# Optimization experiments

Measured on AMD Instinct MI355X. Metric: run time of the kernel, lower is better.

Reference implementation:

```python
import jax, jax.numpy as jnp
import numpy as np

N_Q, N_X, N_Z = 1024, 512, 512
N_PER = N_Q + N_X + N_Z        # 2048 nodes per graph
B = 16                          # graphs per batch
DEG = 16                        # avg in/out degree
E_PER = N_PER * DEG
N = B * N_PER                   # 32768 total nodes
E = B * E_PER                   # 524288 total edges
HID, HEADS, L = 128, 4, 3
DH = HID // HEADS               # 32 per-head dim
EPS = 1e-5


def setup_inputs() -> dict:
    key = jax.random.key(0)
    ks = jax.random.split(key, 10)
    # one-hot node-type features (qubit / X-stab / Z-stab), tiled over batch
    sn = jnp.zeros((N_PER, 3), jnp.float32)
    sn = sn.at[:N_Q, 0].set(1.0).at[N_Q:N_Q + N_X, 1].set(1.0).at[N_Q + N_X:, 2].set(1.0)
    x = jnp.tile(sn, (B, 1))  # [N,3]
    # random sparse edges, graph-local then offset (mimics dense_to_sparse + Batch)
    src = jax.random.randint(ks[0], (B, E_PER), 0, N_PER)
    dst = jax.random.randint(ks[1], (B, E_PER), 0, N_PER)
    off = (jnp.arange(B) * N_PER)[:, None]
    edge_src = (src + off).reshape(-1).astype(jnp.int32)
    edge_dst = (dst + off).reshape(-1).astype(jnp.int32)
    seg = jnp.repeat(jnp.arange(B, dtype=jnp.int32), N_PER)  # graph id per node
    s = 0.05
    return dict(
        x=x, edge_src=edge_src, edge_dst=edge_dst, seg=seg,
        in_w=jax.random.normal(ks[2], (3, HID)) * s, in_b=jnp.zeros((HID,)),
        qw=jax.random.normal(ks[3], (L, HID, HID)) * s, qb=jnp.zeros((L, HID)),
        kw=jax.random.normal(ks[4], (L, HID, HID)) * s, kb=jnp.zeros((L, HID)),
        vw=jax.random.normal(ks[5], (L, HID, HID)) * s, vb=jnp.zeros((L, HID)),
        sw=jax.random.normal(ks[6], (L, HID, HID)) * s, sb=jnp.zeros((L, HID)),
        fw=jax.random.normal(ks[7], (L, HID, HID)) * s, fb=jnp.zeros((L, HID)),
        ln_g=jnp.ones((L, HID)), ln_b=jnp.zeros((L, HID)),
    )


def _layer_norm(h, g, b):
    mu = jnp.mean(h, axis=-1, keepdims=True)
    var = jnp.mean(jnp.square(h - mu), axis=-1, keepdims=True)
    return (h - mu) * jax.lax.rsqrt(var + EPS) * g + b


def reference(x, edge_src, edge_dst, seg, in_w, in_b, qw, qb, kw, kb, vw, vb,
              sw, sb, fw, fb, ln_g, ln_b):
    scale = 1.0 / jnp.sqrt(jnp.float32(DH))
    h = x @ in_w + in_b  # [N,HID]
    for i in range(L):
        h_res = h
        # TransformerConv: per-edge multi-head attention (softmax over in-neighbors)
        q = (h @ qw[i] + qb[i]).reshape(N, HEADS, DH)
        k = (h @ kw[i] + kb[i]).reshape(N, HEADS, DH)
        v = (h @ vw[i] + vb[i]).reshape(N, HEADS, DH)
        logits = jnp.einsum('ehd,ehd->eh', q[edge_dst], k[edge_src]) * scale  # [E,H]
        m = jax.ops.segment_max(logits, edge_dst, num_segments=N)             # [N,H]
        e = jnp.exp(logits - m[edge_dst])
        z = jax.ops.segment_sum(e, edge_dst, num_segments=N)                  # [N,H]
        alpha = e / z[edge_dst]
        agg = jax.ops.segment_sum(alpha[:, :, None] * v[edge_src], edge_dst,
                                  num_segments=N).reshape(N, HID)
        h = agg + h @ sw[i] + sb[i]        # root/skip linear (root_weight=True)
        # dropout is a no-op in eval mode
        h = h + jax.nn.relu(h @ fw[i] + fb[i])   # FFN residual
        h = h + h_res                            # outer residual
        h = jax.nn.relu(_layer_norm(h, ln_g[i], ln_b[i]))
    # global_mean_pool over graphs
    tot = jax.ops.segment_sum(h, seg, num_segments=B)                       # [B,HID]
    cnt = jax.ops.segment_sum(jnp.ones((N, 1), h.dtype), seg, num_segments=B)
    return tot / cnt
```

## Files before the change

kernel.cpp:

```cpp
#include <hip/hip_runtime.h>
#include <hip/hip_bf16.h>

#define N_TOT 32768
#define E_TOT 524288
#define HID 128
#define B_GR 16
#define NPER 2048
#define LAYERS 3
#define EPSLN 1e-5f
#define ELLW 64
#define SCALE_L2E (0.17677669529663687f * 1.4426950408889634f)

typedef float f4 __attribute__((ext_vector_type(4)));
typedef short bf16x8 __attribute__((ext_vector_type(8)));
typedef unsigned short u16x4 __attribute__((ext_vector_type(4)));

__device__ __forceinline__ unsigned short f2bf_rne(float x) {
    unsigned u = __float_as_uint(x);
    unsigned r = (u + 0x7FFFu + ((u >> 16) & 1u)) >> 16;
    return (unsigned short)r;
}

__device__ __forceinline__ float bf2f(unsigned short u) {
    return __uint_as_float(((unsigned)u) << 16);
}

__device__ __forceinline__ void unpack8(uint4 w, float* f) {
    f[0] = __uint_as_float(w.x << 16); f[1] = __uint_as_float(w.x & 0xFFFF0000u);
    f[2] = __uint_as_float(w.y << 16); f[3] = __uint_as_float(w.y & 0xFFFF0000u);
    f[4] = __uint_as_float(w.z << 16); f[5] = __uint_as_float(w.z & 0xFFFF0000u);
    f[6] = __uint_as_float(w.w << 16); f[7] = __uint_as_float(w.w & 0xFFFF0000u);
}

__global__ __launch_bounds__(256) void k_zp(const float* __restrict__ qw, const float* __restrict__ kw,
                                            const float* __restrict__ vw, const float* __restrict__ sw,
                                            const float* __restrict__ fw, unsigned short* __restrict__ wt,
                                            int* __restrict__ cursor, float* __restrict__ outz) {
    if (blockIdx.x < 960) {
        int mid = blockIdx.x >> 6;
        int within = (blockIdx.x & 63) * 256 + threadIdx.x;
        int l = mid / 5, t = mid % 5;
        const float* src = (t == 0 ? qw : t == 1 ? kw : t == 2 ? vw : t == 3 ? sw : fw) + l * HID * HID;
        int c = within >> 7;
        int kk = within & 127;
        int k = kk ^ ((c & 7) << 3);
        float sc = (t == 0) ? SCALE_L2E : 1.0f;
        wt[mid * HID * HID + c * HID + kk] = f2bf_rne(src[k * HID + c] * sc);
    } else if (blockIdx.x < 992) {
        int i = (blockIdx.x - 960) * 256 + threadIdx.x;
        reinterpret_cast<int4*>(cursor)[i] = int4{0, 0, 0, 0};
    } else {
        f4 z4 = {0.f, 0.f, 0.f, 0.f};
        reinterpret_cast<f4*>(outz)[threadIdx.x * 2] = z4;
        reinterpret_cast<f4*>(outz)[threadIdx.x * 2 + 1] = z4;
    }
}

#define GEMM_COMPUTE_G(acc, AL, WG)                                                         \
    {                                                                                       \
        _Pragma("unroll")                                                                   \
        for (int ks = 0; ks < 4; ++ks) {                                                    \
            bf16x8 a0 = *reinterpret_cast<const bf16x8*>(                                   \
                &AL[wm * 32 + lr][(ks * 32 + lg * 8) ^ swz]);                               \
            bf16x8 a1 = *reinterpret_cast<const bf16x8*>(                                   \
                &AL[wm * 32 + 16 + lr][(ks * 32 + lg * 8) ^ swz]);                          \
            _Pragma("unroll")                                                               \
            for (int n = 0; n < 4; ++n) {                                                   \
                bf16x8 b = *reinterpret_cast<const bf16x8*>(                                \
                    (WG) + (wn * 64 + n * 16 + lr) * HID + ((ks * 32 + lg * 8) ^ swz));     \
                acc[0][n] = __builtin_amdgcn_mfma_f32_16x16x32_bf16(a0, b, acc[0][n], 0, 0, 0); \
                acc[1][n] = __builtin_amdgcn_mfma_f32_16x16x32_bf16(a1, b, acc[1][n], 0, 0, 0); \
            }                                                                               \
        }                                                                                   \
    }

#define ZERO_ACC(acc)                                                        \
    {                                                                        \
        _Pragma("unroll")                                                    \
        for (int m = 0; m < 2; ++m)                                          \
            _Pragma("unroll")                                                \
            for (int n = 0; n < 4; ++n) acc[m][n] = f4{0, 0, 0, 0};          \
    }

#define QKV_EPILOGUE(ACC, T_IDX)                                                            \
    {                                                                                       \
        _Pragma("unroll")                                                                   \
        for (int n = 0; n < 4; ++n) {                                                       \
            int col = wn * 64 + n * 16 + lr;                                                \
            float bs = biases[T_IDX][col];                                                  \
            if (T_IDX == 0) bs *= SCALE_L2E;                                                \
            unsigned short* outp = (T_IDX == 0) ? oq : okv + ((T_IDX == 2) ? 128 : 0);      \
            const size_t stride = (T_IDX == 0) ? HID : 256;                                 \
            _Pragma("unroll")                                                               \
            for (int m = 0; m < 2; ++m) {                                                   \
                _Pragma("unroll")                                                           \
                for (int r = 0; r < 4; ++r) {                                               \
                    int row = r0 + wm * 32 + m * 16 + lg * 4 + r;                           \
                    outp[(size_t)row * stride + col] = f2bf_rne(ACC[m][n][r] + bs);         \
                }                                                                           \
            }                                                                               \
        }                                                                                   \
    }

__global__ __launch_bounds__(256) void k_scatter_init(const int* __restrict__ esrc, const int* __restrict__ edst,
                                                      int* __restrict__ cursor, unsigned short* __restrict__ ell,
                                                      const float* __restrict__ x,
                                                      const float* __restrict__ in_w,
                                                      const float* __restrict__ in_b,
                                                      const unsigned short* __restrict__ wl,
                                                      const float* __restrict__ qb, const float* __restrict__ kb,
                                                      const float* __restrict__ vb,
                                                      unsigned short* __restrict__ h16,
                                                      unsigned short* __restrict__ oq,
                                                      unsigned short* __restrict__ okv) {
    __shared__ unsigned short A_lds[64][HID];
    int tid = threadIdx.x;
    if (blockIdx.x < E_TOT / 256) {
        int e = blockIdx.x * 256 + tid;
        int d = edst[e];
        int pos = atomicAdd(&cursor[d], 1);
        if (pos < ELLW) ell[d * ELLW + pos] = (unsigned short)esrc[e];
        return;
    }
    int r0 = (blockIdx.x - E_TOT / 256) * 64;
    int lane = tid & 63, w = tid >> 6;
    int wm = w >> 1, wn = w & 1;
    int lr = lane & 15, lg = lane >> 4;
    int swz = (lane & 7) << 3;

    #pragma unroll
    for (int p = 0; p < 8; ++p) {
        int idx = p * 256 + tid;
        int row = idx >> 5;
        int k0 = (idx & 31) * 4;
        int n = r0 + row;
        float x0 = x[n * 3 + 0], x1 = x[n * 3 + 1], x2 = x[n * 3 + 2];
        u16x4 b;
        #pragma unroll
        for (int i = 0; i < 4; ++i) {
            int c = k0 + i;
            b[i] = f2bf_rne(x0 * in_w[c] + x1 * in_w[HID + c] + x2 * in_w[2 * HID + c] + in_b[c]);
        }
        int cs = k0 ^ ((row & 7) << 3);
        *reinterpret_cast<u16x4*>(&A_lds[row][cs]) = b;
        *reinterpret_cast<u16x4*>(&h16[(size_t)n * HID + cs]) = b;
    }
    __syncthreads();

    const float* biases[3] = {qb, kb, vb};
    f4 acc[2][4];
    #pragma unroll
    for (int t = 0; t < 3; ++t) {
        ZERO_ACC(acc);
        GEMM_COMPUTE_G(acc, A_lds, wl + t * HID * HID);
        QKV_EPILOGUE(acc, t);
    }
}

__global__ __launch_bounds__(256) void k_attn5(const unsigned short* __restrict__ qb16,
                                               const unsigned short* __restrict__ kv16,
                                               const int* __restrict__ deg,
                                               const unsigned short* __restrict__ ell,
                                               unsigned short* __restrict__ outagg) {
    int bid = blockIdx.x;
    int xcd = bid & 7;
    int chunk = bid >> 3;
    int g2 = xcd + 8 * (chunk >> 9);
    int nb = g2 * 512 + (chunk & 511);
    int n = nb * 4 + (threadIdx.x >> 6);

    int lane = threadIdx.x & 63;
    int g = lane >> 4, l = lane & 15;
    int dg = deg[n];
    if (dg > ELLW) dg = ELLW;
    const unsigned short* eb = ell + n * ELLW;

    float qf[8];
    {
        uint4 qw = *reinterpret_cast<const uint4*>(&qb16[(size_t)n * HID + l * 8]);
        unpack8(qw, qf);
    }

    float z = 0.f;
    float a[8] = {0, 0, 0, 0, 0, 0, 0, 0};
    int nit = (dg + 3) >> 2;
    if (nit > 0) {
        int j = g;
        bool val = j < dg;
        int sj = val ? (int)eb[j] : 0;
        const unsigned short* kv = kv16 + (size_t)sj * 256 + l * 8;
        uint4 kw = *reinterpret_cast<const uint4*>(kv);
        uint4 vw = *reinterpret_cast<const uint4*>(kv + 128);
        for (int it = 0; it < nit; ++it) {
            int jn = j + 4;
            bool valn = jn < dg;
            int sn = valn ? (int)eb[jn] : 0;
            const unsigned short* kvn = kv16 + (size_t)sn * 256 + l * 8;
            uint4 kwn = *reinterpret_cast<const uint4*>(kvn);
            uint4 vwn = *reinterpret_cast<const uint4*>(kvn + 128);
            float kf[8]; unpack8(kw, kf);
            float d = qf[0] * kf[0] + qf[1] * kf[1] + qf[2] * kf[2] + qf[3] * kf[3] +
                      qf[4] * kf[4] + qf[5] * kf[5] + qf[6] * kf[6] + qf[7] * kf[7];
            d += __shfl_xor(d, 1);
            d += __shfl_xor(d, 2);
            float p = val ? exp2f(d) : 0.f;
            z += p;
            float vf[8]; unpack8(vw, vf);
            #pragma unroll
            for (int c = 0; c < 8; ++c) a[c] += p * vf[c];
            kw = kwn; vw = vwn; j = jn; val = valn;
        }
    }
    #pragma unroll
    for (int off = 16; off <= 32; off <<= 1) {
        z += __shfl_xor(z, off);
        #pragma unroll
        for (int c = 0; c < 8; ++c) a[c] += __shfl_xor(a[c], off);
    }
    if (g == 0) {
        float inv = (z > 0.f) ? 1.f / z : 0.f;
        uint4 o;
        o.x = (unsigned)f2bf_rne(a[0] * inv) | ((unsigned)f2bf_rne(a[1] * inv) << 16);
        o.y = (unsigned)f2bf_rne(a[2] * inv) | ((unsigned)f2bf_rne(a[3] * inv) << 16);
        o.z = (unsigned)f2bf_rne(a[4] * inv) | ((unsigned)f2bf_rne(a[5] * inv) << 16);
        o.w = (unsigned)f2bf_rne(a[6] * inv) | ((unsigned)f2bf_rne(a[7] * inv) << 16);
        *reinterpret_cast<uint4*>(&outagg[(size_t)n * HID + l * 8]) = o;
    }
}

template <bool QKV>
__global__ __launch_bounds__(256) void k_fused(const unsigned short* __restrict__ h16,
                                               const unsigned short* __restrict__ wsf,
                                               const float* __restrict__ sb,
                                               const float* __restrict__ fb,
                                               const unsigned short* __restrict__ agg16,
                                               const float* __restrict__ gma,
                                               const float* __restrict__ beta,
                                               unsigned short* __restrict__ out16,
                                               const unsigned short* __restrict__ wqkv,
                                               const float* __restrict__ qb2,
                                               const float* __restrict__ kb2,
                                               const float* __restrict__ vb2,
                                               unsigned short* __restrict__ oq,
                                               unsigned short* __restrict__ okv,
                                               float* __restrict__ pool_out) {
    __shared__ unsigned short A_lds[64][HID];
    __shared__ float RS[64][4];

    int tid = threadIdx.x;
    int r0 = blockIdx.x * 64;
    int lane = tid & 63, w = tid >> 6;
    int wm = w >> 1, wn = w & 1;
    int lr = lane & 15, lg = lane >> 4;
    int swz = (lane & 7) << 3;

    {
        const uint4* hs = reinterpret_cast<const uint4*>(h16 + (size_t)r0 * HID);
        #pragma unroll
        for (int p = 0; p < 4; ++p)
            reinterpret_cast<uint4*>(&A_lds[0][0])[p * 256 + tid] = hs[p * 256 + tid];
    }
    __syncthreads();
    f4 acc[2][4];
    ZERO_ACC(acc);
    GEMM_COMPUTE_G(acc, A_lds, wsf);
    __syncthreads();

    unsigned short hres[2][4][4];
    #pragma unroll
    for (int n = 0; n < 4; ++n) {
        int col = wn * 64 + n * 16 + lr;
        float bs = sb[col];
        #pragma unroll
        for (int m = 0; m < 2; ++m) {
            #pragma unroll
            for (int r = 0; r < 4; ++r) {
                int rl = wm * 32 + m * 16 + lg * 4 + r;
                int cs = col ^ ((rl & 7) << 3);
                hres[m][n][r] = A_lds[rl][cs];
                float v = acc[m][n][r] + bs + bf2f(agg16[(size_t)(r0 + rl) * HID + col]);
                acc[m][n][r] = v;
                A_lds[rl][cs] = f2bf_rne(v);
            }
        }
    }
    __syncthreads();
    f4 acc2[2][4];
    ZERO_ACC(acc2);
    GEMM_COMPUTE_G(acc2, A_lds, wsf + HID * HID);

    #pragma unroll
    for (int n = 0; n < 4; ++n) {
        int col = wn * 64 + n * 16 + lr;
        float bs = fb[col];
        #pragma unroll
        for (int m = 0; m < 2; ++m) {
            #pragma unroll
            for (int r = 0; r < 4; ++r) {
                acc[m][n][r] = acc[m][n][r] + fmaxf(acc2[m][n][r] + bs, 0.f) + bf2f(hres[m][n][r]);
            }
        }
    }
    #pragma unroll
    for (int m = 0; m < 2; ++m) {
        #pragma unroll
        for (int r = 0; r < 4; ++r) {
            float s = acc[m][0][r] + acc[m][1][r] + acc[m][2][r] + acc[m][3][r];
            float ss = acc[m][0][r] * acc[m][0][r] + acc[m][1][r] * acc[m][1][r] +
                       acc[m][2][r] * acc[m][2][r] + acc[m][3][r] * acc[m][3][r];
            #pragma unroll
            for (int off = 1; off < 16; off <<= 1) {
                s += __shfl_xor(s, off);
                ss += __shfl_xor(ss, off);
            }
            if (lr == 0) {
                int rl = wm * 32 + m * 16 + lg * 4 + r;
                RS[rl][wn * 2] = s;
                RS[rl][wn * 2 + 1] = ss;
            }
        }
    }
    __syncthreads();

    float g_[4], b_[4];
    #pragma unroll
    for (int n = 0; n < 4; ++n) {
        int col = wn * 64 + n * 16 + lr;
        g_[n] = gma[col];
        b_[n] = beta[col];
    }
    #pragma unroll
    for (int m = 0; m < 2; ++m) {
        #pragma unroll
        for (int r = 0; r < 4; ++r) {
            int rl = wm * 32 + m * 16 + lg * 4 + r;
            float sum = RS[rl][0] + RS[rl][2];
            float ssum = RS[rl][1] + RS[rl][3];
            float mu = sum * (1.f / 128.f);
            float var = ssum * (1.f / 128.f) - mu * mu;
            float rsq = rsqrtf(fmaxf(var, 0.f) + EPSLN);
            int rs = (rl & 7) << 3;
            #pragma unroll
            for (int n = 0; n < 4; ++n) {
                int col = wn * 64 + n * 16 + lr;
                float y = (acc[m][n][r] - mu) * rsq * g_[n] + b_[n];
                A_lds[rl][col ^ rs] = f2bf_rne(fmaxf(y, 0.f));
            }
        }
    }
    __syncthreads();

    if (QKV) {
        {
            uint4* hd = reinterpret_cast<uint4*>(out16 + (size_t)r0 * HID);
            #pragma unroll
            for (int p = 0; p < 4; ++p)
                hd[p * 256 + tid] = reinterpret_cast<const uint4*>(&A_lds[0][0])[p * 256 + tid];
        }
        const float* biases[3] = {qb2, kb2, vb2};
        f4 acc3[2][4];
        #pragma unroll
        for (int t = 0; t < 3; ++t) {
            ZERO_ACC(acc3);
            GEMM_COMPUTE_G(acc3, A_lds, wqkv + t * HID * HID);
            QKV_EPILOGUE(acc3, t);
        }
    } else {
        if (tid < HID) {
            float s2 = 0.f;
            #pragma unroll 8
            for (int r = 0; r < 64; ++r) s2 += bf2f(A_lds[r][tid ^ ((r & 7) << 3)]);
            atomicAdd(&pool_out[(r0 >> 11) * HID + tid], s2 * (1.f / NPER));
        }
    }
}

extern "C" void kernel_launch(void* const* d_in, const int* in_sizes, int n_in,
                              void* d_out, int out_size, void* d_ws, size_t ws_size,
                              hipStream_t stream) {
    const float* x    = (const float*)d_in[0];
    const int*   esrc = (const int*)d_in[1];
    const int*   edst = (const int*)d_in[2];
    const float* in_w = (const float*)d_in[4];
    const float* in_b = (const float*)d_in[5];
    const float* qw   = (const float*)d_in[6];
    const float* qb   = (const float*)d_in[7];
    const float* kw   = (const float*)d_in[8];
    const float* kb   = (const float*)d_in[9];
    const float* vw   = (const float*)d_in[10];
    const float* vb   = (const float*)d_in[11];
    const float* sw   = (const float*)d_in[12];
    const float* sb   = (const float*)d_in[13];
    const float* fw   = (const float*)d_in[14];
    const float* fb   = (const float*)d_in[15];
    const float* ln_g = (const float*)d_in[16];
    const float* ln_b = (const float*)d_in[17];
    float* out = (float*)d_out;

    const size_t NH = (size_t)N_TOT * HID;
    unsigned short* h16   = (unsigned short*)d_ws;
    unsigned short* agg16 = h16 + NH;
    unsigned short* qb16  = agg16 + NH;
    unsigned short* kv16  = qb16 + NH;
    unsigned short* wt    = kv16 + 2 * NH;
    int* cursor = (int*)(wt + 15 * HID * HID);
    unsigned short* ell = (unsigned short*)(cursor + N_TOT);

    k_zp<<<993, 256, 0, stream>>>(qw, kw, vw, sw, fw, wt, cursor, out);
    k_scatter_init<<<E_TOT / 256 + N_TOT / 64, 256, 0, stream>>>(
        esrc, edst, cursor, ell, x, in_w, in_b, wt, qb, kb, vb, h16, qb16, kv16);

    for (int l = 0; l < LAYERS; ++l) {
        const unsigned short* wt_l = wt + (size_t)l * 5 * HID * HID;
        k_attn5<<<N_TOT / 4, 256, 0, stream>>>(qb16, kv16, cursor, ell, agg16);
        if (l + 1 < LAYERS) {
            const unsigned short* wt_n = wt + (size_t)(l + 1) * 5 * HID * HID;
            k_fused<true><<<N_TOT / 64, 256, 0, stream>>>(
                h16, wt_l + 3 * HID * HID, sb + (size_t)l * HID, fb + (size_t)l * HID,
                agg16, ln_g + (size_t)l * HID, ln_b + (size_t)l * HID, h16,
                wt_n, qb + (size_t)(l + 1) * HID, kb + (size_t)(l + 1) * HID,
                vb + (size_t)(l + 1) * HID, qb16, kv16, nullptr);
        } else {
            k_fused<false><<<N_TOT / 64, 256, 0, stream>>>(
                h16, wt_l + 3 * HID * HID, sb + (size_t)l * HID, fb + (size_t)l * HID,
                agg16, ln_g + (size_t)l * HID, ln_b + (size_t)l * HID, nullptr,
                nullptr, nullptr, nullptr, nullptr, nullptr, nullptr, out);
        }
    }
}
```

Baseline: 174.5 us.

## Build ELL adjacency in LDS per graph slice and stage GEMM weights in LDS

Edge bucketing now happens inside the setup kernel: each block scans one graph's edges, buckets the ones whose destination falls in its 256-node slice using shared-memory atomics, and writes the ELL rows and degrees out contiguously. This replaces global atomics and scattered ELL writes, and removes the separate cursor zeroing. The trade-off is that each graph's edge list is re-read by 8 blocks. All GEMMs now first copy their 128x128 bf16 weight tile into LDS instead of reading B fragments from global or L2. This costs 32KB of extra LDS per block and adds barriers, which may reduce occupancy.

```diff
diff --git a/kernel.cpp b/kernel.cpp
--- a/kernel.cpp
+++ b/kernel.cpp
@@ -9,6 +9,7 @@
 #define LAYERS 3
 #define EPSLN 1e-5f
 #define ELLW 64
+#define E_PER_G (E_TOT / B_GR)
 #define SCALE_L2E (0.17677669529663687f * 1.4426950408889634f)
 
 typedef float f4 __attribute__((ext_vector_type(4)));
@@ -35,10 +36,14 @@
 __global__ __launch_bounds__(256) void k_zp(const float* __restrict__ qw, const float* __restrict__ kw,
                                             const float* __restrict__ vw, const float* __restrict__ sw,
                                             const float* __restrict__ fw, unsigned short* __restrict__ wt,
-                                            int* __restrict__ cursor, float* __restrict__ outz) {
+                                            const int* __restrict__ esrc, const int* __restrict__ edst,
+                                            int* __restrict__ deg, unsigned short* __restrict__ ell,
+                                            float* __restrict__ outz) {
+    __shared__ __align__(16) char smem[33792];
+    int tid = threadIdx.x;
     if (blockIdx.x < 960) {
         int mid = blockIdx.x >> 6;
-        int within = (blockIdx.x & 63) * 256 + threadIdx.x;
+        int within = (blockIdx.x & 63) * 256 + tid;
         int l = mid / 5, t = mid % 5;
         const float* src = (t == 0 ? qw : t == 1 ? kw : t == 2 ? vw : t == 3 ? sw : fw) + l * HID * HID;
         int c = within >> 7;
@@ -46,17 +51,44 @@
         int k = kk ^ ((c & 7) << 3);
         float sc = (t == 0) ? SCALE_L2E : 1.0f;
         wt[mid * HID * HID + c * HID + kk] = f2bf_rne(src[k * HID + c] * sc);
-    } else if (blockIdx.x < 992) {
-        int i = (blockIdx.x - 960) * 256 + threadIdx.x;
-        reinterpret_cast<int4*>(cursor)[i] = int4{0, 0, 0, 0};
+    } else if (blockIdx.x < 1088) {
+        int b = blockIdx.x - 960;
+        int g = b >> 3, q = b & 7;
+        int nbase = g * NPER + q * 256;
+        int* cnt = reinterpret_cast<int*>(smem);
+        unsigned short (*el)[ELLW] = reinterpret_cast<unsigned short (*)[ELLW]>(smem + 1024);
+        cnt[tid] = 0;
+        __syncthreads();
+        const int4* d4 = reinterpret_cast<const int4*>(edst + g * E_PER_G);
+        const int4* s4 = reinterpret_cast<const int4*>(esrc + g * E_PER_G);
+        for (int it = 0; it < E_PER_G / 1024; ++it) {
+            int4 dd = d4[it * 256 + tid];
+            int4 ss = s4[it * 256 + tid];
+            #pragma unroll
+            for (int j = 0; j < 4; ++j) {
+                int dv = (&dd.x)[j];
+                int sv = (&ss.x)[j];
+                unsigned local = (unsigned)(dv - nbase);
+                if (local < 256u) {
+                    int pos = atomicAdd(&cnt[local], 1);
+                    if (pos < ELLW) el[local][pos] = (unsigned short)sv;
+                }
+            }
+        }
+        __syncthreads();
+        uint4* eg = reinterpret_cast<uint4*>(ell + (size_t)nbase * ELLW);
+        const uint4* es = reinterpret_cast<const uint4*>(&el[0][0]);
+        #pragma unroll
+        for (int p = 0; p < 8; ++p) eg[p * 256 + tid] = es[p * 256 + tid];
+        deg[nbase + tid] = cnt[tid];
     } else {
         f4 z4 = {0.f, 0.f, 0.f, 0.f};
-        reinterpret_cast<f4*>(outz)[threadIdx.x * 2] = z4;
-        reinterpret_cast<f4*>(outz)[threadIdx.x * 2 + 1] = z4;
-    }
-}
-
-#define GEMM_COMPUTE_G(acc, AL, WG)                                                         \
+        reinterpret_cast<f4*>(outz)[tid * 2] = z4;
+        reinterpret_cast<f4*>(outz)[tid * 2 + 1] = z4;
+    }
+}
+
+#define GEMM_COMPUTE(acc, AL)                                                               \
     {                                                                                       \
         _Pragma("unroll")                                                                   \
         for (int ks = 0; ks < 4; ++ks) {                                                    \
@@ -67,7 +99,7 @@
             _Pragma("unroll")                                                               \
             for (int n = 0; n < 4; ++n) {                                                   \
                 bf16x8 b = *reinterpret_cast<const bf16x8*>(                                \
-                    (WG) + (wn * 64 + n * 16 + lr) * HID + ((ks * 32 + lg * 8) ^ swz));     \
+                    &W_lds[wn * 64 + n * 16 + lr][(ks * 32 + lg * 8) ^ swz]);               \
                 acc[0][n] = __builtin_amdgcn_mfma_f32_16x16x32_bf16(a0, b, acc[0][n], 0, 0, 0); \
                 acc[1][n] = __builtin_amdgcn_mfma_f32_16x16x32_bf16(a1, b, acc[1][n], 0, 0, 0); \
             }                                                                               \
@@ -80,6 +112,14 @@
         for (int m = 0; m < 2; ++m)                                          \
             _Pragma("unroll")                                                \
             for (int n = 0; n < 4; ++n) acc[m][n] = f4{0, 0, 0, 0};          \
+    }
+
+#define COPY_W(SRC)                                                          \
+    {                                                                        \
+        _Pragma("unroll")                                                    \
+        for (int p = 0; p < 8; ++p)                                          \
+            reinterpret_cast<uint4*>(&W_lds[0][0])[p * 256 + tid] =          \
+                reinterpret_cast<const uint4*>(SRC)[p * 256 + tid];          \
     }
 
 #define QKV_EPILOGUE(ACC, T_IDX)                                                            \
@@ -102,27 +142,19 @@
         }                                                                                   \
     }
 
-__global__ __launch_bounds__(256) void k_scatter_init(const int* __restrict__ esrc, const int* __restrict__ edst,
-                                                      int* __restrict__ cursor, unsigned short* __restrict__ ell,
-                                                      const float* __restrict__ x,
-                                                      const float* __restrict__ in_w,
-                                                      const float* __restrict__ in_b,
-                                                      const unsigned short* __restrict__ wl,
-                                                      const float* __restrict__ qb, const float* __restrict__ kb,
-                                                      const float* __restrict__ vb,
-                                                      unsigned short* __restrict__ h16,
-                                                      unsigned short* __restrict__ oq,
-                                                      unsigned short* __restrict__ okv) {
+__global__ __launch_bounds__(256) void k_init_qkv(const float* __restrict__ x,
+                                                  const float* __restrict__ in_w,
+                                                  const float* __restrict__ in_b,
+                                                  const unsigned short* __restrict__ wl,
+                                                  const float* __restrict__ qb, const float* __restrict__ kb,
+                                                  const float* __restrict__ vb,
+                                                  unsigned short* __restrict__ h16,
+                                                  unsigned short* __restrict__ oq,
+                                                  unsigned short* __restrict__ okv) {
     __shared__ unsigned short A_lds[64][HID];
+    __shared__ unsigned short W_lds[HID][HID];
     int tid = threadIdx.x;
-    if (blockIdx.x < E_TOT / 256) {
-        int e = blockIdx.x * 256 + tid;
-        int d = edst[e];
-        int pos = atomicAdd(&cursor[d], 1);
-        if (pos < ELLW) ell[d * ELLW + pos] = (unsigned short)esrc[e];
-        return;
-    }
-    int r0 = (blockIdx.x - E_TOT / 256) * 64;
+    int r0 = blockIdx.x * 64;
     int lane = tid & 63, w = tid >> 6;
     int wm = w >> 1, wn = w & 1;
     int lr = lane & 15, lg = lane >> 4;
@@ -145,15 +177,17 @@
         *reinterpret_cast<u16x4*>(&A_lds[row][cs]) = b;
         *reinterpret_cast<u16x4*>(&h16[(size_t)n * HID + cs]) = b;
     }
-    __syncthreads();
 
     const float* biases[3] = {qb, kb, vb};
     f4 acc[2][4];
     #pragma unroll
     for (int t = 0; t < 3; ++t) {
+        COPY_W(wl + t * HID * HID);
+        __syncthreads();
         ZERO_ACC(acc);
-        GEMM_COMPUTE_G(acc, A_lds, wl + t * HID * HID);
+        GEMM_COMPUTE(acc, A_lds);
         QKV_EPILOGUE(acc, t);
+        __syncthreads();
     }
 }
 
@@ -245,6 +279,7 @@
                                                unsigned short* __restrict__ okv,
                                                float* __restrict__ pool_out) {
     __shared__ unsigned short A_lds[64][HID];
+    __shared__ unsigned short W_lds[HID][HID];
     __shared__ float RS[64][4];
 
     int tid = threadIdx.x;
@@ -260,10 +295,11 @@
         for (int p = 0; p < 4; ++p)
             reinterpret_cast<uint4*>(&A_lds[0][0])[p * 256 + tid] = hs[p * 256 + tid];
     }
+    COPY_W(wsf);
     __syncthreads();
     f4 acc[2][4];
     ZERO_ACC(acc);
-    GEMM_COMPUTE_G(acc, A_lds, wsf);
+    GEMM_COMPUTE(acc, A_lds);
     __syncthreads();
 
     unsigned short hres[2][4][4];
@@ -284,10 +320,11 @@
             }
         }
     }
+    COPY_W(wsf + HID * HID);
     __syncthreads();
     f4 acc2[2][4];
     ZERO_ACC(acc2);
-    GEMM_COMPUTE_G(acc2, A_lds, wsf + HID * HID);
+    GEMM_COMPUTE(acc2, A_lds);
 
     #pragma unroll
     for (int n = 0; n < 4; ++n) {
@@ -361,9 +398,12 @@
         f4 acc3[2][4];
         #pragma unroll
         for (int t = 0; t < 3; ++t) {
+            COPY_W(wqkv + t * HID * HID);
+            __syncthreads();
             ZERO_ACC(acc3);
-            GEMM_COMPUTE_G(acc3, A_lds, wqkv + t * HID * HID);
+            GEMM_COMPUTE(acc3, A_lds);
             QKV_EPILOGUE(acc3, t);
+            __syncthreads();
         }
     } else {
         if (tid < HID) {
@@ -403,16 +443,15 @@
     unsigned short* qb16  = agg16 + NH;
     unsigned short* kv16  = qb16 + NH;
     unsigned short* wt    = kv16 + 2 * NH;
-    int* cursor = (int*)(wt + 15 * HID * HID);
-    unsigned short* ell = (unsigned short*)(cursor + N_TOT);
-
-    k_zp<<<993, 256, 0, stream>>>(qw, kw, vw, sw, fw, wt, cursor, out);
-    k_scatter_init<<<E_TOT / 256 + N_TOT / 64, 256, 0, stream>>>(
-        esrc, edst, cursor, ell, x, in_w, in_b, wt, qb, kb, vb, h16, qb16, kv16);
+    int* deg = (int*)(wt + 15 * HID * HID);
+    unsigned short* ell = (unsigned short*)(deg + N_TOT);
+
+    k_zp<<<1089, 256, 0, stream>>>(qw, kw, vw, sw, fw, wt, esrc, edst, deg, ell, out);
+    k_init_qkv<<<N_TOT / 64, 256, 0, stream>>>(x, in_w, in_b, wt, qb, kb, vb, h16, qb16, kv16);
 
     for (int l = 0; l < LAYERS; ++l) {
         const unsigned short* wt_l = wt + (size_t)l * 5 * HID * HID;
-        k_attn5<<<N_TOT / 4, 256, 0, stream>>>(qb16, kv16, cursor, ell, agg16);
+        k_attn5<<<N_TOT / 4, 256, 0, stream>>>(qb16, kv16, deg, ell, agg16);
         if (l + 1 < LAYERS) {
             const unsigned short* wt_n = wt + (size_t)(l + 1) * 5 * HID * HID;
             k_fused<true><<<N_TOT / 64, 256, 0, stream>>>(
```

After: 162.0 us. 7.2% less time.
